# Optimization experiments

Hardware: AMD Instinct MI355X
Metric: run time of the kernel (lower is better)

## Reference

```python
import jax, jax.numpy as jnp
import numpy as np

SOS = 4998
EOS = 4999
SCALING = 2.0


def setup_inputs() -> dict:
    key = jax.random.key(0)
    ks = jax.random.split(key, 12)
    B, T, E, D, A, C, F, ODIM, L = 32, 1000, 512, 1024, 512, 10, 100, 5000, 100
    s = 0.02
    return {
        "hpad": jax.random.normal(ks[0], (B, T, E), jnp.float32),
        "ys": jax.random.randint(ks[1], (B, L), 0, SOS, jnp.int32),
        # AttLoc params
        "w_enc": jax.random.normal(ks[2], (A, E), jnp.float32) * s,
        "b_enc": jnp.zeros((A,), jnp.float32),
        "w_dec": jax.random.normal(ks[3], (A, D), jnp.float32) * s,
        "w_att": jax.random.normal(ks[4], (A, C), jnp.float32) * s,
        "w_conv": jax.random.normal(ks[5], (C, 1, 2 * F + 1), jnp.float32) * s,  # OIH 1D conv kernel
        "w_gvec": jax.random.normal(ks[6], (1, A), jnp.float32) * s,
        "b_gvec": jnp.zeros((1,), jnp.float32),
        # Decoder params
        "embed": jax.random.normal(ks[7], (ODIM, D), jnp.float32) * s,
        "w_ih": jax.random.normal(ks[8], (4 * D, D + E), jnp.float32) * s,
        "w_hh": jax.random.normal(ks[9], (4 * D, D), jnp.float32) * s,
        "b_ih": jnp.zeros((4 * D,), jnp.float32),
        "b_hh": jnp.zeros((4 * D,), jnp.float32),
        "w_out": jax.random.normal(ks[10], (ODIM, D), jnp.float32) * s,
        "b_out": jnp.zeros((ODIM,), jnp.float32),
    }


def _decode(hpad, ys, w_enc, b_enc, w_dec, w_att, w_conv, w_gvec, b_gvec,
            embed, w_ih, w_hh, b_ih, b_hh, w_out, b_out):
    B, T, E = hpad.shape
    D = w_hh.shape[1]
    F = (w_conv.shape[-1] - 1) // 2
    # ys_in = [sos; y] per utterance (all same length -> already padded)
    ys_in = jnp.concatenate([jnp.full((B, 1), SOS, ys.dtype), ys], axis=1)  # [B, olen]
    eys = embed[ys_in]                                                      # [B, olen, D]
    # pre_compute_enc_h = mlp_enc(enc_h)
    pre = jnp.einsum('bte,ae->bta', hpad, w_enc) + b_enc                    # [B, T, A]
    att0 = jnp.full((B, T), 1.0 / T, hpad.dtype)   # uniform init attention (all hlen == T)
    z0 = jnp.zeros((B, D), hpad.dtype)
    c0 = jnp.zeros((B, D), hpad.dtype)

    def step(carry, ey_i):
        z, c, aw = carry
        # location-aware conv over previous attention weights: [B,1,T] -> [B,C,T]
        conv = jax.lax.conv_general_dilated(aw[:, None, :], w_conv, (1,), [(F, F)],
                                            dimension_numbers=('NCH', 'OIH', 'NCH'))
        att_feat = jnp.einsum('bct,ac->bta', conv, w_att)                   # mlp_att
        dec = (z @ w_dec.T)[:, None, :]                                     # mlp_dec, tiled
        e = jnp.tanh(att_feat + pre + dec) @ w_gvec[0] + b_gvec[0]          # [B, T]
        w = jax.nn.softmax(SCALING * e, axis=1)
        ctx = jnp.einsum('bt,bte->be', w, hpad)                             # [B, E]
        # LSTMCell
        x = jnp.concatenate([ey_i, ctx], axis=1)                            # [B, D+E]
        gates = x @ w_ih.T + b_ih + z @ w_hh.T + b_hh
        i_g, f_g, g_g, o_g = jnp.split(gates, 4, axis=1)
        c_new = jax.nn.sigmoid(f_g) * c + jax.nn.sigmoid(i_g) * jnp.tanh(g_g)
        z_new = jax.nn.sigmoid(o_g) * jnp.tanh(c_new)
        return (z_new, c_new, w), z_new

    _, z_all = jax.lax.scan(step, (z0, c0, att0), jnp.swapaxes(eys, 0, 1))  # [olen, B, D]
    y_all = jnp.einsum('obd,vd->obv', z_all, w_out) + b_out                 # [olen, B, odim]
    return jnp.swapaxes(y_all, 0, 1)                                        # [B, olen, odim]


def reference(hpad, ys, w_enc, b_enc, w_dec, w_att, w_conv, w_gvec, b_gvec,
              embed, w_ih, w_hh, b_ih, b_hh, w_out, b_out):
    return _decode(hpad, ys, w_enc, b_enc, w_dec, w_att, w_conv, w_gvec, b_gvec,
                   embed, w_ih, w_hh, b_ih, b_hh, w_out, b_out)
```

## Files before the change

kernel.cpp:

```cpp
#include <hip/hip_runtime.h>
#include <math.h>

#define B_    32
#define T_    1000
#define E_    512
#define D_    1024
#define A_    512
#define C_    10
#define F_    100
#define ODIM_ 5000
#define OLEN_ 101
#define SOS_  4998

#define OFF_PRE   0u
#define N_PREF    (32u*512u*1000u/2u)
#define OFF_HPB   (OFF_PRE + N_PREF)
#define N_HPBF    (32u*1000u*512u/2u)
#define OFF_PP    (OFF_HPB + N_HPBF)
#define N_PP      (32u*512u*16u)
#define OFF_AW    (OFF_PP + N_PP)
#define N_AW1     (32u*1000u)
#define N_AW      (2u*N_AW1)
#define OFF_S     (OFF_AW + N_AW)
#define N_S       (64u)
#define OFF_CTX   (OFF_S + N_S)
#define N_CTX     (32u*512u)
#define OFF_GP    (OFF_CTX + N_CTX)
#define N_GP      (8u*32u*4096u)
#define OFF_Z     (OFF_GP + N_GP)
#define N_Z1      (32u*1024u)
#define OFF_C     (OFF_Z + N_Z1)
#define OFF_ZALL  (OFF_C + N_Z1)

__device__ __forceinline__ float fast_tanh(float x) {
    float cx = fminf(8.f, fmaxf(-8.f, x));
    float e = __expf(2.f * cx);
    return (e - 1.f) * __builtin_amdgcn_rcpf(e + 1.f);
}
__device__ __forceinline__ float fast_sigmoid(float x) {
    float cx = fminf(30.f, fmaxf(-30.f, x));
    return __builtin_amdgcn_rcpf(1.f + __expf(-cx));
}

__device__ __forceinline__ unsigned bf16rne(float f) {
    unsigned u = __float_as_uint(f);
    return (u + 0x7fffu + ((u >> 16) & 1u)) >> 16;
}
__device__ __forceinline__ unsigned packbf(float lo, float hi) {
    return bf16rne(lo) | (bf16rne(hi) << 16);
}
__device__ __forceinline__ float bflo(unsigned u) { return __uint_as_float(u << 16); }
__device__ __forceinline__ float bfhi(unsigned u) { return __uint_as_float(u & 0xffff0000u); }

__global__ __launch_bounds__(256) void k_init(const float* __restrict__ watt,
                                              const float* __restrict__ gvec,
                                              float* ws) {
    int i = blockIdx.x * 256 + threadIdx.x;
    if (i < (int)N_Z1) { ws[OFF_Z + i] = 0.f; ws[OFF_C + i] = 0.f; }
    if (i < (int)N_CTX) ws[OFF_CTX + i] = 0.f;
    if (i < (int)N_AW) ws[OFF_AW + i] = 1.0f;
    if (i < 64) ws[OFF_S + i] = 1000.f;
    if (i < 16384) {
        int a = i & 511;
        float* d = ws + OFF_PP + (size_t)i * 16;
        #pragma unroll
        for (int c = 0; c < 10; ++c) d[c] = watt[a * 10 + c];
        d[10] = gvec[a];
        d[11] = 0.f; d[12] = 0.f; d[13] = 0.f; d[14] = 0.f; d[15] = 0.f;
    }
}

__global__ __launch_bounds__(256) void k_hp16(const float* __restrict__ hp, float* ws) {
    uint2* hpb = (uint2*)(ws + OFF_HPB);
    const float4* src = (const float4*)hp;
    for (unsigned i = blockIdx.x * 256 + threadIdx.x; i < 4096000u; i += 4000u * 256u) {
        float4 v = src[i];
        uint2 o;
        o.x = packbf(v.x, v.y);
        o.y = packbf(v.z, v.w);
        hpb[i] = o;
    }
}

__global__ __launch_bounds__(256) void k_pre_t(const float* __restrict__ hp,
                                               const float* __restrict__ we,
                                               const float* __restrict__ be,
                                               float* ws) {
    __shared__ float As[64][68];
    __shared__ float Bs[64][68];
    unsigned short* preb = (unsigned short*)(ws + OFF_PRE);
    int bt = blockIdx.y;
    int b = bt >> 4, tc = bt & 15;
    int t0 = tc * 64;
    int n0 = blockIdx.x * 64;
    int tid = threadIdx.x;
    int tr = tid >> 4, tcl = tid & 15;
    float acc[4][4] = {};
    for (int k0 = 0; k0 < 512; k0 += 64) {
        for (int i = tid; i < 1024; i += 256) {
            int m = i >> 4, kq = (i & 15) << 2;
            int t = t0 + m;
            float4 v = (t < 1000) ? *(const float4*)&hp[((size_t)(b * 1000 + t)) * 512 + k0 + kq]
                                  : make_float4(0.f, 0.f, 0.f, 0.f);
            As[kq + 0][m] = v.x; As[kq + 1][m] = v.y; As[kq + 2][m] = v.z; As[kq + 3][m] = v.w;
            float4 w = *(const float4*)&we[(size_t)(n0 + m) * 512 + k0 + kq];
            Bs[kq + 0][m] = w.x; Bs[kq + 1][m] = w.y; Bs[kq + 2][m] = w.z; Bs[kq + 3][m] = w.w;
        }
        __syncthreads();
        #pragma unroll 16
        for (int kk = 0; kk < 64; ++kk) {
            float4 av = *(const float4*)&As[kk][tr << 2];
            float4 bv = *(const float4*)&Bs[kk][tcl << 2];
            float a[4] = {av.x, av.y, av.z, av.w};
            float bq[4] = {bv.x, bv.y, bv.z, bv.w};
            #pragma unroll
            for (int i = 0; i < 4; i++)
                #pragma unroll
                for (int j = 0; j < 4; j++) acc[i][j] += a[i] * bq[j];
        }
        __syncthreads();
    }
    int tt = t0 + (tr << 2);
    if (tt < 1000) {
        #pragma unroll
        for (int j = 0; j < 4; ++j) {
            int a = n0 + (tcl << 2) + j;
            float bea = be[a];
            uint2 o;
            o.x = packbf(acc[0][j] + bea, acc[1][j] + bea);
            o.y = packbf(acc[2][j] + bea, acc[3][j] + bea);
            *(uint2*)&preb[((size_t)(b * 512 + a)) * 1000 + tt] = o;
        }
    }
}

__global__ __launch_bounds__(256, 2) void k_prep(const float* __restrict__ wdec,
                                                 const float* __restrict__ wih,
                                                 const float* __restrict__ whh,
                                                 const float* __restrict__ embed,
                                                 const int* __restrict__ ys,
                                                 float* ws, int step) {
    __shared__ float wlds[32][132];
    __shared__ float xs[32][36];
    int tid = threadIdx.x;
    if (blockIdx.x < 256) {
        if (blockIdx.x < 64) ws[OFF_CTX + blockIdx.x * 256 + tid] = 0.f;
        if (blockIdx.x == 64 && tid < 32) ws[OFF_S + (step & 1) * 32 + tid] = 0.f;
        int blk = blockIdx.x;
        int nt = blk & 31, ks = blk >> 5;
        int n0 = nt * 128;
        bool isE = (ks < 4);
        int kloc = isE ? ks * 256 : (ks - 4) * 256;
        int r = tid >> 1, h = tid & 1;
        int bx = tid >> 3, q8 = tid & 7;
        int tok = (step == 0) ? SOS_ : ys[bx * 100 + step - 1];
        const float* xsrc = isE ? (embed + (size_t)tok * 1024 + kloc)
                                : (ws + OFF_Z + (size_t)bx * 1024 + kloc);
        int nq = tid & 31, bq = tid >> 5;
        float acc[4][4] = {};
        for (int kc = 0; kc < 8; ++kc) {
            int koff = kc * 32;
            {
                const float* wrow = isE ? (wih + (size_t)(n0 + r) * 1536 + kloc + koff + h * 16)
                                        : (whh + (size_t)(n0 + r) * 1024 + kloc + koff + h * 16);
                #pragma unroll
                for (int j = 0; j < 4; ++j) {
                    float4 v = *(const float4*)&wrow[j * 4];
                    int kb = h * 16 + j * 4;
                    wlds[kb + 0][r] = v.x; wlds[kb + 1][r] = v.y;
                    wlds[kb + 2][r] = v.z; wlds[kb + 3][r] = v.w;
                }
            }
            {
                float4 v = *(const float4*)&xsrc[koff + q8 * 4];
                xs[q8 * 4 + 0][bx] = v.x; xs[q8 * 4 + 1][bx] = v.y;
                xs[q8 * 4 + 2][bx] = v.z; xs[q8 * 4 + 3][bx] = v.w;
            }
            __syncthreads();
            #pragma unroll 8
            for (int kk = 0; kk < 32; ++kk) {
                float4 wv = *(const float4*)&wlds[kk][nq * 4];
                float4 xv = *(const float4*)&xs[kk][bq * 4];
                float wa[4] = {wv.x, wv.y, wv.z, wv.w};
                float xa[4] = {xv.x, xv.y, xv.z, xv.w};
                #pragma unroll
                for (int i = 0; i < 4; i++)
                    #pragma unroll
                    for (int j = 0; j < 4; j++) acc[i][j] += wa[i] * xa[j];
            }
            __syncthreads();
        }
        float* gp = ws + OFF_GP + (size_t)(ks * 32 + bq * 4) * 4096 + n0 + nq * 4;
        #pragma unroll
        for (int j = 0; j < 4; j++)
            #pragma unroll
            for (int i = 0; i < 4; i++)
                gp[(size_t)j * 4096 + i] = acc[i][j];
    } else {
        int blk = blockIdx.x - 256;
        int nt = blk & 3, ks = blk >> 2;
        int n0 = nt * 128;
        int kloc = ks * 256;
        int r = tid >> 1, h = tid & 1;
        int bx = tid >> 3, q8 = tid & 7;
        const float* xsrc = ws + OFF_Z + (size_t)bx * 1024 + kloc;
        int nq = tid & 31, bq = tid >> 5;
        float acc[4][4] = {};
        for (int kc = 0; kc < 8; ++kc) {
            int koff = kc * 32;
            {
                const float* wrow = wdec + (size_t)(n0 + r) * 1024 + kloc + koff + h * 16;
                #pragma unroll
                for (int j = 0; j < 4; ++j) {
                    float4 v = *(const float4*)&wrow[j * 4];
                    int kb = h * 16 + j * 4;
                    wlds[kb + 0][r] = v.x; wlds[kb + 1][r] = v.y;
                    wlds[kb + 2][r] = v.z; wlds[kb + 3][r] = v.w;
                }
            }
            {
                float4 v = *(const float4*)&xsrc[koff + q8 * 4];
                xs[q8 * 4 + 0][bx] = v.x; xs[q8 * 4 + 1][bx] = v.y;
                xs[q8 * 4 + 2][bx] = v.z; xs[q8 * 4 + 3][bx] = v.w;
            }
            __syncthreads();
            #pragma unroll 8
            for (int kk = 0; kk < 32; ++kk) {
                float4 wv = *(const float4*)&wlds[kk][nq * 4];
                float4 xv = *(const float4*)&xs[kk][bq * 4];
                float wa[4] = {wv.x, wv.y, wv.z, wv.w};
                float xa[4] = {xv.x, xv.y, xv.z, xv.w};
                #pragma unroll
                for (int i = 0; i < 4; i++)
                    #pragma unroll
                    for (int j = 0; j < 4; j++) acc[i][j] += wa[i] * xa[j];
            }
            __syncthreads();
        }
        #pragma unroll
        for (int j = 0; j < 4; j++)
            #pragma unroll
            for (int i = 0; i < 4; i++) {
                int b = bq * 4 + j, a = n0 + nq * 4 + i;
                ws[OFF_PP + ((size_t)(b * 512 + a)) * 16 + 11 + ks] = acc[i][j];
            }
    }
}

__global__ __launch_bounds__(512, 2) void k_ectx(const float* __restrict__ wconv,
                                                 const float* __restrict__ bgv,
                                                 float* ws, int step) {
    __shared__ float part[1024];
    __shared__ float wsh[128];
    __shared__ float awn[332];
    __shared__ float wcv[2016];
    __shared__ float cls[1280];
    const unsigned short* preb = (const unsigned short*)(ws + OFF_PRE);
    const unsigned short* hpb  = (const unsigned short*)(ws + OFF_HPB);
    int b = blockIdx.x >> 3, tc = blockIdx.x & 7;
    int tbase = tc * 128;
    int tid = threadIdx.x;
    const float* awprev = ws + OFF_AW + ((step + 1) & 1) * N_AW1;
    float*       awcur  = ws + OFF_AW + (step & 1) * N_AW1;
    if (tid < 332) {
        float invS = __builtin_amdgcn_rcpf(ws[OFF_S + ((step + 1) & 1) * 32 + b]);
        int g = tbase - 100 + tid;
        awn[tid] = (g >= 0 && g < 1000) ? awprev[b * 1000 + g] * invS : 0.f;
    }
    for (int i = tid; i < 2010; i += 512) wcv[i] = wconv[i];
    __syncthreads();
    if (tid < 320) {
        int c = tid >> 5, tq = tid & 31;
        int base = tq * 4;
        const float* wc = wcv + c * 201;
        float a0 = awn[base], a1 = awn[base + 1], a2 = awn[base + 2], a3 = awn[base + 3];
        float c0 = 0.f, c1 = 0.f, c2 = 0.f, c3 = 0.f;
        #pragma unroll 4
        for (int j = 0; j < 201; ++j) {
            float w = wc[j];
            c0 += a0 * w; c1 += a1 * w; c2 += a2 * w; c3 += a3 * w;
            a0 = a1; a1 = a2; a2 = a3;
            a3 = awn[base + 4 + j];
        }
        *(float4*)&cls[c * 128 + base] = make_float4(c0, c1, c2, c3);
    }
    __syncthreads();
    int w = tid >> 6, l = tid & 63;
    int wu = __builtin_amdgcn_readfirstlane(w);
    int t = tbase + l * 2;
    bool valid = (t < 1000);
    float2 cvv[10];
    #pragma unroll
    for (int c = 0; c < 10; ++c)
        cvv[c] = valid ? make_float2(cls[c * 128 + l * 2], cls[c * 128 + l * 2 + 1])
                       : make_float2(0.f, 0.f);
    const float* pb = ws + OFF_PP + ((size_t)(b * 512 + wu * 64)) * 16;
    const unsigned short* pt = preb + ((size_t)(b * 512 + wu * 64)) * 1000 + t;
    float ex = 0.f, ey = 0.f;
    #pragma unroll 8
    for (int i = 0; i < 64; ++i) {
        unsigned u = valid ? *(const unsigned*)pt : 0u;
        pt += 1000;
        float4 q0 = *(const float4*)(pb + i * 16);
        float4 q1 = *(const float4*)(pb + i * 16 + 4);
        float4 q2 = *(const float4*)(pb + i * 16 + 8);
        float4 q3 = *(const float4*)(pb + i * 16 + 12);
        float dec = q2.w + q3.x + q3.y + q3.z;
        float px = bflo(u), py = bfhi(u);
        float sx = px + dec, sy = py + dec;
        sx += cvv[0].x * q0.x; sy += cvv[0].y * q0.x;
        sx += cvv[1].x * q0.y; sy += cvv[1].y * q0.y;
        sx += cvv[2].x * q0.z; sy += cvv[2].y * q0.z;
        sx += cvv[3].x * q0.w; sy += cvv[3].y * q0.w;
        sx += cvv[4].x * q1.x; sy += cvv[4].y * q1.x;
        sx += cvv[5].x * q1.y; sy += cvv[5].y * q1.y;
        sx += cvv[6].x * q1.z; sy += cvv[6].y * q1.z;
        sx += cvv[7].x * q1.w; sy += cvv[7].y * q1.w;
        sx += cvv[8].x * q2.x; sy += cvv[8].y * q2.x;
        sx += cvv[9].x * q2.y; sy += cvv[9].y * q2.y;
        ex += q2.z * fast_tanh(sx);
        ey += q2.z * fast_tanh(sy);
    }
    part[w * 128 + l * 2]     = ex;
    part[w * 128 + l * 2 + 1] = ey;
    __syncthreads();
    float wtil = 0.f;
    if (tid < 128) {
        int tt = tbase + tid;
        float e = 0.f;
        #pragma unroll
        for (int j = 0; j < 8; ++j) e += part[j * 128 + tid];
        if (tt < 1000) {
            wtil = __expf(2.f * (e + bgv[0]));
            awcur[b * 1000 + tt] = wtil;
        }
        wsh[tid] = wtil;
    }
    __syncthreads();
    if (tid < 128) {
        float ss = wtil;
        #pragma unroll
        for (int off = 32; off > 0; off >>= 1) ss += __shfl_xor(ss, off, 64);
        if ((tid & 63) == 0) part[tid >> 6] = ss;
    }
    __syncthreads();
    if (tid == 0) atomicAdd(&ws[OFF_S + (step & 1) * 32 + b], part[0] + part[1]);
    int e4 = tid & 127, th = tid >> 7;
    int lt0 = th * 32;
    int ltend = lt0 + 32;
    int tmax = 1000 - tbase; if (ltend > tmax) ltend = tmax;
    float4 acc = make_float4(0.f, 0.f, 0.f, 0.f);
    for (int lt = lt0; lt < ltend; ++lt) {
        float wv = wsh[lt];
        uint2 hu = *(const uint2*)&hpb[((size_t)(b * 1000 + tbase + lt)) * 512 + e4 * 4];
        acc.x += wv * bflo(hu.x); acc.y += wv * bfhi(hu.x);
        acc.z += wv * bflo(hu.y); acc.w += wv * bfhi(hu.y);
    }
    float* cx = ws + OFF_CTX + b * 512 + e4 * 4;
    atomicAdd(cx + 0, acc.x); atomicAdd(cx + 1, acc.y);
    atomicAdd(cx + 2, acc.z); atomicAdd(cx + 3, acc.w);
}

__global__ __launch_bounds__(256, 2) void k_gl(const float* __restrict__ wih,
                                               const float* __restrict__ bih,
                                               const float* __restrict__ bhh,
                                               float* ws, int step) {
    __shared__ float wlds[32][20];
    __shared__ float xs[32][33];
    __shared__ float glb[16][33];
    __shared__ float sinv[32];
    int tid = threadIdx.x;
    int d0 = blockIdx.x * 4;
    if (tid < 32) sinv[tid] = __builtin_amdgcn_rcpf(ws[OFF_S + (step & 1) * 32 + tid]);
    __syncthreads();
    int r = tid >> 4, h = tid & 15;
    int ng_r = (r >> 2) * 1024 + d0 + (r & 3);
    const float* wrow = wih + (size_t)ng_r * 1536 + 1024 + h * 2;
    int bx = tid >> 3, q8 = tid & 7;
    const float* xsrc = ws + OFF_CTX + (size_t)bx * 512 + q8 * 4;
    float xscale = sinv[bx];
    int nq = tid & 7, bq = tid >> 3;
    float acc[2] = {0.f, 0.f};
    for (int kc = 0; kc < 16; ++kc) {
        int k0 = kc * 32;
        {
            float2 v = *(const float2*)&wrow[k0];
            wlds[h * 2 + 0][r] = v.x;
            wlds[h * 2 + 1][r] = v.y;
        }
        {
            float4 v = *(const float4*)&xsrc[k0];
            xs[q8 * 4 + 0][bx] = v.x * xscale; xs[q8 * 4 + 1][bx] = v.y * xscale;
            xs[q8 * 4 + 2][bx] = v.z * xscale; xs[q8 * 4 + 3][bx] = v.w * xscale;
        }
        __syncthreads();
        #pragma unroll 8
        for (int kk = 0; kk < 32; ++kk) {
            float w0 = wlds[kk][nq * 2], w1 = wlds[kk][nq * 2 + 1];
            float x  = xs[kk][bq];
            acc[0] += w0 * x;
            acc[1] += w1 * x;
        }
        __syncthreads();
    }
    #pragma unroll
    for (int i = 0; i < 2; ++i) {
        int nl = nq * 2 + i;
        int ng = (nl >> 2) * 1024 + d0 + (nl & 3);
        float s = acc[i] + bih[ng] + bhh[ng];
        #pragma unroll
        for (int sl = 0; sl < 8; ++sl)
            s += ws[OFF_GP + (size_t)(sl * 32 + bq) * 4096 + ng];
        glb[nl][bq] = s;
    }
    __syncthreads();
    if (tid < 128) {
        int dl = tid >> 5, b = tid & 31;
        float gi = glb[dl][b];
        float gf = glb[4 + dl][b];
        float gg = glb[8 + dl][b];
        float go = glb[12 + dl][b];
        int id = b * 1024 + d0 + dl;
        float c_old = ws[OFF_C + id];
        float si = fast_sigmoid(gi);
        float sf = fast_sigmoid(gf);
        float so = fast_sigmoid(go);
        float cn = sf * c_old + si * fast_tanh(gg);
        float hh = so * fast_tanh(cn);
        ws[OFF_C + id] = cn;
        ws[OFF_Z + id] = hh;
        ws[OFF_ZALL + ((size_t)step * 32 + b) * 1024 + d0 + dl] = hh;
    }
}

__global__ __launch_bounds__(256) void k_out(const float* __restrict__ zall,
                                             const float* __restrict__ wo,
                                             const float* __restrict__ bo,
                                             float* __restrict__ out) {
    __shared__ float As[16][132];
    __shared__ float Bs[16][132];
    int m0 = blockIdx.y * 128, n0 = blockIdx.x * 128;
    int tid = threadIdx.x;
    int tx = tid & 15, ty = tid >> 4;
    float acc[8][8] = {};
    int ar = tid >> 1, ah = (tid & 1) * 8;
    for (int k0 = 0; k0 < 1024; k0 += 16) {
        {
            int gm = m0 + ar;
            float4 a0, a1;
            if (gm < 3232) {
                a0 = *(const float4*)&zall[(size_t)gm * 1024 + k0 + ah];
                a1 = *(const float4*)&zall[(size_t)gm * 1024 + k0 + ah + 4];
            } else { a0 = a1 = make_float4(0.f, 0.f, 0.f, 0.f); }
            As[ah + 0][ar] = a0.x; As[ah + 1][ar] = a0.y; As[ah + 2][ar] = a0.z; As[ah + 3][ar] = a0.w;
            As[ah + 4][ar] = a1.x; As[ah + 5][ar] = a1.y; As[ah + 6][ar] = a1.z; As[ah + 7][ar] = a1.w;
            int gn = n0 + ar;
            float4 b0, b1;
            if (gn < 5000) {
                b0 = *(const float4*)&wo[(size_t)gn * 1024 + k0 + ah];
                b1 = *(const float4*)&wo[(size_t)gn * 1024 + k0 + ah + 4];
            } else { b0 = b1 = make_float4(0.f, 0.f, 0.f, 0.f); }
            Bs[ah + 0][ar] = b0.x; Bs[ah + 1][ar] = b0.y; Bs[ah + 2][ar] = b0.z; Bs[ah + 3][ar] = b0.w;
            Bs[ah + 4][ar] = b1.x; Bs[ah + 5][ar] = b1.y; Bs[ah + 6][ar] = b1.z; Bs[ah + 7][ar] = b1.w;
        }
        __syncthreads();
        #pragma unroll
        for (int kk = 0; kk < 16; ++kk) {
            float4 a0v = *(const float4*)&As[kk][ty * 8];
            float4 a1v = *(const float4*)&As[kk][ty * 8 + 4];
            float4 b0v = *(const float4*)&Bs[kk][tx * 8];
            float4 b1v = *(const float4*)&Bs[kk][tx * 8 + 4];
            float am[8] = {a0v.x, a0v.y, a0v.z, a0v.w, a1v.x, a1v.y, a1v.z, a1v.w};
            float bn[8] = {b0v.x, b0v.y, b0v.z, b0v.w, b1v.x, b1v.y, b1v.z, b1v.w};
            #pragma unroll
            for (int i = 0; i < 8; i++)
                #pragma unroll
                for (int j = 0; j < 8; j++) acc[i][j] += am[i] * bn[j];
        }
        __syncthreads();
    }
    #pragma unroll
    for (int i = 0; i < 8; i++) {
        int m = m0 + ty * 8 + i;
        if (m >= 3232) continue;
        int b = m & 31, o = m >> 5;
        #pragma unroll
        for (int j = 0; j < 8; j++) {
            int v = n0 + tx * 8 + j;
            if (v < 5000)
                out[((size_t)b * 101 + o) * 5000 + v] = acc[i][j] + bo[v];
        }
    }
}

extern "C" void kernel_launch(void* const* d_in, const int* in_sizes, int n_in,
                              void* d_out, int out_size, void* d_ws, size_t ws_size,
                              hipStream_t stream) {
    const float* hpad   = (const float*)d_in[0];
    const int*   ys     = (const int*)d_in[1];
    const float* w_enc  = (const float*)d_in[2];
    const float* b_enc  = (const float*)d_in[3];
    const float* w_dec  = (const float*)d_in[4];
    const float* w_att  = (const float*)d_in[5];
    const float* w_conv = (const float*)d_in[6];
    const float* w_gvec = (const float*)d_in[7];
    const float* b_gvec = (const float*)d_in[8];
    const float* embed  = (const float*)d_in[9];
    const float* w_ih   = (const float*)d_in[10];
    const float* w_hh   = (const float*)d_in[11];
    const float* b_ih   = (const float*)d_in[12];
    const float* b_hh   = (const float*)d_in[13];
    const float* w_out  = (const float*)d_in[14];
    const float* b_out  = (const float*)d_in[15];
    float* ws  = (float*)d_ws;
    float* out = (float*)d_out;

    k_init<<<256, 256, 0, stream>>>(w_att, w_gvec, ws);
    k_hp16<<<4000, 256, 0, stream>>>(hpad, ws);
    k_pre_t<<<dim3(8, 512), 256, 0, stream>>>(hpad, w_enc, b_enc, ws);

    for (int step = 0; step < OLEN_; ++step) {
        k_prep<<<272, 256, 0, stream>>>(w_dec, w_ih, w_hh, embed, ys, ws, step);
        k_ectx<<<256, 512, 0, stream>>>(w_conv, b_gvec, ws, step);
        k_gl<<<256, 256, 0, stream>>>(w_ih, b_ih, b_hh, ws, step);
    }

    k_out<<<dim3(40, 26), 256, 0, stream>>>(ws + OFF_ZALL, w_out, b_out, out);
}
```

Before: 10.86 ms.

## Move location-conv computation from attention kernel into prep kernel blocks

The location-aware convolution over the previous attention weights is taken out of k_ectx and computed by 320 extra blocks of k_prep, one per (batch, channel) pair. Results go to a new global buffer that k_ectx reads directly. This removes the LDS staging, the conv loop and two barriers from the attention/context kernel, which may free LDS and shorten its critical path. Because the conv now finishes before k_ectx overwrites the weights, the attention buffer is no longer double-buffered. The cost is an extra global write and read of the conv output, plus a larger prep launch whose conv blocks do strided, uncoalesced loads.

```diff
diff --git a/kernel.cpp b/kernel.cpp
--- a/kernel.cpp
+++ b/kernel.cpp
@@ -18,9 +18,10 @@
 #define N_HPBF    (32u*1000u*512u/2u)
 #define OFF_PP    (OFF_HPB + N_HPBF)
 #define N_PP      (32u*512u*16u)
-#define OFF_AW    (OFF_PP + N_PP)
-#define N_AW1     (32u*1000u)
-#define N_AW      (2u*N_AW1)
+#define OFF_CONV  (OFF_PP + N_PP)
+#define N_CONVB   (32u*10u*1000u)
+#define OFF_AW    (OFF_CONV + N_CONVB)
+#define N_AW      (32u*1000u)
 #define OFF_S     (OFF_AW + N_AW)
 #define N_S       (64u)
 #define OFF_CTX   (OFF_S + N_S)
@@ -59,7 +60,7 @@
     if (i < (int)N_Z1) { ws[OFF_Z + i] = 0.f; ws[OFF_C + i] = 0.f; }
     if (i < (int)N_CTX) ws[OFF_CTX + i] = 0.f;
     if (i < (int)N_AW) ws[OFF_AW + i] = 1.0f;
-    if (i < 64) ws[OFF_S + i] = 1000.f;
+    if (i < 64) ws[OFF_S + i] = (i >= 32) ? 1000.f : 0.f;
     if (i < 16384) {
         int a = i & 511;
         float* d = ws + OFF_PP + (size_t)i * 16;
@@ -135,6 +136,7 @@
 }
 
 __global__ __launch_bounds__(256, 2) void k_prep(const float* __restrict__ wdec,
+                                                 const float* __restrict__ wconv,
                                                  const float* __restrict__ wih,
                                                  const float* __restrict__ whh,
                                                  const float* __restrict__ embed,
@@ -196,8 +198,32 @@
             #pragma unroll
             for (int i = 0; i < 4; i++)
                 gp[(size_t)j * 4096 + i] = acc[i][j];
+    } else if (blockIdx.x < 576) {
+        int blk = blockIdx.x - 256;
+        int b = blk / 10, c = blk - b * 10;
+        if (tid >= 250) return;
+        float invS = __builtin_amdgcn_rcpf(ws[OFF_S + ((step + 1) & 1) * 32 + b]);
+        int t = tid * 4;
+        const float* ar = ws + OFF_AW + b * 1000;
+        const float* wc = wconv + c * 201;
+        float a0, a1, a2, a3;
+        a0 = (t - 100 >= 0) ? ar[t - 100] : 0.f;
+        a1 = (t -  99 >= 0) ? ar[t -  99] : 0.f;
+        a2 = (t -  98 >= 0) ? ar[t -  98] : 0.f;
+        a3 = (t -  97 >= 0) ? ar[t -  97] : 0.f;
+        float c0 = 0.f, c1 = 0.f, c2 = 0.f, c3 = 0.f;
+        #pragma unroll 4
+        for (int j = 0; j < 201; ++j) {
+            float w = wc[j];
+            c0 += a0 * w; c1 += a1 * w; c2 += a2 * w; c3 += a3 * w;
+            a0 = a1; a1 = a2; a2 = a3;
+            int ni = t + j - 96;
+            a3 = (ni >= 0 && ni < 1000) ? ar[ni] : 0.f;
+        }
+        float* o = ws + OFF_CONV + (size_t)(b * 10 + c) * 1000 + t;
+        o[0] = c0 * invS; o[1] = c1 * invS; o[2] = c2 * invS; o[3] = c3 * invS;
     } else {
-        int blk = blockIdx.x - 256;
+        int blk = blockIdx.x - 576;
         int nt = blk & 3, ks = blk >> 2;
         int n0 = nt * 128;
         int kloc = ks * 256;
@@ -247,53 +273,24 @@
     }
 }
 
-__global__ __launch_bounds__(512, 2) void k_ectx(const float* __restrict__ wconv,
-                                                 const float* __restrict__ bgv,
+__global__ __launch_bounds__(512, 2) void k_ectx(const float* __restrict__ bgv,
                                                  float* ws, int step) {
     __shared__ float part[1024];
     __shared__ float wsh[128];
-    __shared__ float awn[332];
-    __shared__ float wcv[2016];
-    __shared__ float cls[1280];
     const unsigned short* preb = (const unsigned short*)(ws + OFF_PRE);
     const unsigned short* hpb  = (const unsigned short*)(ws + OFF_HPB);
     int b = blockIdx.x >> 3, tc = blockIdx.x & 7;
     int tbase = tc * 128;
     int tid = threadIdx.x;
-    const float* awprev = ws + OFF_AW + ((step + 1) & 1) * N_AW1;
-    float*       awcur  = ws + OFF_AW + (step & 1) * N_AW1;
-    if (tid < 332) {
-        float invS = __builtin_amdgcn_rcpf(ws[OFF_S + ((step + 1) & 1) * 32 + b]);
-        int g = tbase - 100 + tid;
-        awn[tid] = (g >= 0 && g < 1000) ? awprev[b * 1000 + g] * invS : 0.f;
-    }
-    for (int i = tid; i < 2010; i += 512) wcv[i] = wconv[i];
-    __syncthreads();
-    if (tid < 320) {
-        int c = tid >> 5, tq = tid & 31;
-        int base = tq * 4;
-        const float* wc = wcv + c * 201;
-        float a0 = awn[base], a1 = awn[base + 1], a2 = awn[base + 2], a3 = awn[base + 3];
-        float c0 = 0.f, c1 = 0.f, c2 = 0.f, c3 = 0.f;
-        #pragma unroll 4
-        for (int j = 0; j < 201; ++j) {
-            float w = wc[j];
-            c0 += a0 * w; c1 += a1 * w; c2 += a2 * w; c3 += a3 * w;
-            a0 = a1; a1 = a2; a2 = a3;
-            a3 = awn[base + 4 + j];
-        }
-        *(float4*)&cls[c * 128 + base] = make_float4(c0, c1, c2, c3);
-    }
-    __syncthreads();
     int w = tid >> 6, l = tid & 63;
     int wu = __builtin_amdgcn_readfirstlane(w);
     int t = tbase + l * 2;
     bool valid = (t < 1000);
     float2 cvv[10];
+    const float* convb = ws + OFF_CONV + b * 10000;
     #pragma unroll
     for (int c = 0; c < 10; ++c)
-        cvv[c] = valid ? make_float2(cls[c * 128 + l * 2], cls[c * 128 + l * 2 + 1])
-                       : make_float2(0.f, 0.f);
+        cvv[c] = valid ? *(const float2*)&convb[c * 1000 + t] : make_float2(0.f, 0.f);
     const float* pb = ws + OFF_PP + ((size_t)(b * 512 + wu * 64)) * 16;
     const unsigned short* pt = preb + ((size_t)(b * 512 + wu * 64)) * 1000 + t;
     float ex = 0.f, ey = 0.f;
@@ -332,7 +329,7 @@
         for (int j = 0; j < 8; ++j) e += part[j * 128 + tid];
         if (tt < 1000) {
             wtil = __expf(2.f * (e + bgv[0]));
-            awcur[b * 1000 + tt] = wtil;
+            ws[OFF_AW + b * 1000 + tt] = wtil;
         }
         wsh[tid] = wtil;
     }
@@ -515,13 +512,13 @@
     float* ws  = (float*)d_ws;
     float* out = (float*)d_out;
 
-    k_init<<<256, 256, 0, stream>>>(w_att, w_gvec, ws);
+    k_init<<<128, 256, 0, stream>>>(w_att, w_gvec, ws);
     k_hp16<<<4000, 256, 0, stream>>>(hpad, ws);
     k_pre_t<<<dim3(8, 512), 256, 0, stream>>>(hpad, w_enc, b_enc, ws);
 
     for (int step = 0; step < OLEN_; ++step) {
-        k_prep<<<272, 256, 0, stream>>>(w_dec, w_ih, w_hh, embed, ys, ws, step);
-        k_ectx<<<256, 512, 0, stream>>>(w_conv, b_gvec, ws, step);
+        k_prep<<<592, 256, 0, stream>>>(w_dec, w_conv, w_ih, w_hh, embed, ys, ws, step);
+        k_ectx<<<256, 512, 0, stream>>>(b_gvec, ws, step);
         k_gl<<<256, 256, 0, stream>>>(w_ih, b_ih, b_hh, ws, step);
     }
 
```

Result: slower. 11.17 ms (+2.9%).
